# Performance work log

Hardware: AMD Instinct MI355X
Metric: run time of the kernel (lower is better)

## Reference

```python
import jax, jax.numpy as jnp
import numpy as np

N_NODES = 50000
N_EDGES = 640000
NFEAT = 128
NHID = 128
BN_EPS = 1e-5
GIN_EPS = 0.0  # GINConv default eps


def setup_inputs() -> dict:
    key = jax.random.key(0)
    ks = jax.random.split(key, 8)
    x = jax.random.normal(ks[0], (N_NODES, NFEAT), dtype=jnp.float32)
    edge_index = jax.random.randint(ks[1], (2, N_EDGES), 0, N_NODES, dtype=jnp.int64)
    # xavier-uniform linears, zero bias (per weights_init); BN gamma=1, beta=0
    def xavier(k, fan_in, fan_out):
        a = float(np.sqrt(6.0 / (fan_in + fan_out)))
        return jax.random.uniform(k, (fan_in, fan_out), dtype=jnp.float32, minval=-a, maxval=a)
    W1 = xavier(ks[2], NFEAT, NHID)
    b1 = jnp.zeros((NHID,), dtype=jnp.float32)
    gamma = jnp.ones((NHID,), dtype=jnp.float32)
    beta = jnp.zeros((NHID,), dtype=jnp.float32)
    W2 = xavier(ks[3], NHID, NHID)
    b2 = jnp.zeros((NHID,), dtype=jnp.float32)
    return {"x": x, "edge_index": edge_index, "W1": W1, "b1": b1,
            "gamma": gamma, "beta": beta, "W2": W2, "b2": b2}


def reference(x, edge_index, W1, b1, gamma, beta, W2, b2):
    src, dst = edge_index[0], edge_index[1]
    # sparse neighbor sum-aggregation: agg[i] = sum_{(src->dst=i)} x[src]
    agg = jax.ops.segment_sum(x[src], dst, num_segments=x.shape[0])
    h = (1.0 + GIN_EPS) * x + agg
    # MLP: Linear -> ReLU -> BatchNorm1d (training-mode batch stats) -> Linear
    h = jax.nn.relu(h @ W1 + b1)
    mean = jnp.mean(h, axis=0)
    var = jnp.mean(jnp.square(h - mean), axis=0)  # biased var, as torch BN uses
    h = (h - mean) * jax.lax.rsqrt(var + BN_EPS) * gamma + beta
    return h @ W2 + b2
```

## Files before the change

kernel.cpp:

```cpp
#include <hip/hip_runtime.h>
#include <hip/hip_fp16.h>

#define NNODES 50000
#define NEDGES 640000
#define NF 128
#define XB 3125
#define BINS 196
#define BINCAP 4096
#define P1B 157

typedef __attribute__((ext_vector_type(8))) _Float16 f16x8;
typedef __attribute__((ext_vector_type(4))) float f32x4;

__global__ __launch_bounds__(256) void k_prep(const float* __restrict__ x,
                                              const float* __restrict__ W1,
                                              unsigned short* __restrict__ xh,
                                              _Float16* __restrict__ wp1,
                                              int* __restrict__ gcursor,
                                              float* __restrict__ stats) {
  const int bid = blockIdx.x, t = threadIdx.x;
  if (bid < XB) {
    int i = bid * 256 + t;
    const float4 a = ((const float4*)x)[2 * i];
    const float4 b = ((const float4*)x)[2 * i + 1];
    __half2 h0 = __float22half2_rn(make_float2(a.x, a.y));
    __half2 h1 = __float22half2_rn(make_float2(a.z, a.w));
    __half2 h2 = __float22half2_rn(make_float2(b.x, b.y));
    __half2 h3 = __float22half2_rn(make_float2(b.z, b.w));
    uint4 v;
    v.x = *(unsigned*)&h0; v.y = *(unsigned*)&h1;
    v.z = *(unsigned*)&h2; v.w = *(unsigned*)&h3;
    ((uint4*)xh)[i] = v;
    if (bid == 0) {
      stats[t] = 0.f;
      stats[256 + t] = 0.f;
      if (t < BINS) gcursor[t] = 0;
    }
  } else {
    int f = (bid - XB) * 256 + t;
    int j = f & 7, lane = (f >> 3) & 63, cf = (f >> 9) & 7, ks = f >> 12;
    int k = ks * 32 + ((lane >> 4) << 3) + j;
    int n = cf * 16 + (lane & 15);
    float w = W1[k * NF + n];
    _Float16 hi = (_Float16)w;
    _Float16 lo = (_Float16)(w - (float)hi);
    wp1[f] = hi;
    wp1[16384 + f] = lo;
  }
}

__global__ __launch_bounds__(256) void k_p1(const int* __restrict__ ei,
                                            int* __restrict__ gcursor,
                                            unsigned* __restrict__ binbuf) {
  __shared__ int lcnt[BINS], lbase[BINS];
  const int t = threadIdx.x;
  const int e0 = blockIdx.x * 4096;
  const int n = min(4096, NEDGES - e0);
  if (t < BINS) lcnt[t] = 0;
  __syncthreads();
  for (int i = t; i < n; i += 256)
    atomicAdd(&lcnt[ei[NEDGES + e0 + i] >> 8], 1);
  __syncthreads();
  if (t < BINS) {
    lbase[t] = atomicAdd(&gcursor[t], lcnt[t]);
    lcnt[t] = 0;
  }
  __syncthreads();
  for (int i = t; i < n; i += 256) {
    int s = ei[e0 + i];
    int d = ei[NEDGES + e0 + i];
    int bin = d >> 8;
    int pos = atomicAdd(&lcnt[bin], 1);
    int idx = lbase[bin] + pos;
    if (idx < BINCAP)
      binbuf[bin * BINCAP + idx] = ((unsigned)(d & 255) << 16) | (unsigned)s;
  }
}

__global__ __launch_bounds__(256) void k_p2(const unsigned* __restrict__ binbuf,
                                            const int* __restrict__ gcursor,
                                            int* __restrict__ begdeg,
                                            unsigned short* __restrict__ slot) {
  __shared__ int cnt2[256], pst[256];
  __shared__ unsigned short stg[BINCAP];
  const int t = threadIdx.x;
  const int b = blockIdx.x;
  const int base = b * BINCAP;
  const int nb = min(gcursor[b], BINCAP);
  cnt2[t] = 0;
  __syncthreads();
  for (int i = t; i < nb; i += 256)
    atomicAdd(&cnt2[binbuf[base + i] >> 16], 1);
  __syncthreads();
  pst[t] = cnt2[t];
  __syncthreads();
  for (int d = 1; d < 256; d <<= 1) {
    int u = (t >= d) ? pst[t - d] : 0;
    __syncthreads();
    pst[t] += u;
    __syncthreads();
  }
  pst[t] -= cnt2[t];
  int node = (b << 8) + t;
  if (node < NNODES)
    begdeg[node] = ((base + pst[t]) << 8) | min(cnt2[t], 255);
  cnt2[t] = 0;
  __syncthreads();
  for (int i = t; i < nb; i += 256) {
    unsigned p = binbuf[base + i];
    int dl = p >> 16;
    int pos = atomicAdd(&cnt2[dl], 1);
    stg[pst[dl] + pos] = (unsigned short)(p & 0xffffu);
  }
  __syncthreads();
  for (int i = t; i < nb; i += 256) slot[base + i] = stg[i];
}

__device__ inline void add8h(float* a, uint4 v) {
  const __half2* p = (const __half2*)&v;
#pragma unroll
  for (int q = 0; q < 4; ++q) {
    float2 f = __half22float2(p[q]);
    a[2 * q] += f.x;
    a[2 * q + 1] += f.y;
  }
}

__global__ __launch_bounds__(256) void k_gather(const unsigned short* __restrict__ xh,
                                                const int* __restrict__ begdeg,
                                                const unsigned short* __restrict__ slot,
                                                _Float16* __restrict__ h) {
  const int t = threadIdx.x;
  const int wv = t >> 6, l = t & 63;
  const int node = blockIdx.x * 4 + wv;
  if (node >= NNODES) return;
  const int cg = (l & 15) << 3;
  const int e = l >> 4;
  const int bd = begdeg[node];
  const int beg = bd >> 8;
  const int end = beg + (bd & 255);
  float a[8] = {0.f, 0.f, 0.f, 0.f, 0.f, 0.f, 0.f, 0.f};
  float b[8] = {0.f, 0.f, 0.f, 0.f, 0.f, 0.f, 0.f, 0.f};
  int j = beg + e;
  for (; j + 4 < end; j += 8) {
    const uint4 v0 = *(const uint4*)(xh + (size_t)slot[j] * NF + cg);
    const uint4 v1 = *(const uint4*)(xh + (size_t)slot[j + 4] * NF + cg);
    add8h(a, v0);
    add8h(b, v1);
  }
  if (j < end) {
    const uint4 v0 = *(const uint4*)(xh + (size_t)slot[j] * NF + cg);
    add8h(a, v0);
  }
#pragma unroll
  for (int q = 0; q < 8; ++q) a[q] += b[q];
#pragma unroll
  for (int q = 0; q < 8; ++q) {
    a[q] += __shfl_xor(a[q], 16);
    a[q] += __shfl_xor(a[q], 32);
  }
  if (e == 0) {
    const uint4 sv = *(const uint4*)(xh + (size_t)node * NF + cg);
    add8h(a, sv);
    f16x8 o;
#pragma unroll
    for (int q = 0; q < 8; ++q) o[q] = (_Float16)a[q];
    *(f16x8*)(h + (size_t)node * NF + cg) = o;
  }
}

template <int MODE>
__global__ __launch_bounds__(256, 2) void k_gemm(const _Float16* __restrict__ A,
                                                 const _Float16* __restrict__ wprep,
                                                 const float* __restrict__ bias,
                                                 float* __restrict__ stats,
                                                 _Float16* __restrict__ outh,
                                                 float* __restrict__ outf) {
  __shared__ _Float16 wl[32768];
  __shared__ float red[2][4][128];

  const int t = threadIdx.x;
  const int wv = t >> 6;
  const int l = t & 63;
  const int wrow0 = blockIdx.x * 128 + wv * 16;

  f16x8 areg[2][4];
#pragma unroll
  for (int m = 0; m < 2; ++m) {
    const int arow = wrow0 + m * 64 + (l & 15);
    const bool okA = arow < NNODES;
#pragma unroll
    for (int ks = 0; ks < 4; ++ks) {
      if (okA) {
        areg[m][ks] = *(const f16x8*)(A + (size_t)arow * NF + ks * 32 + ((l >> 4) << 3));
      } else {
        areg[m][ks] = (f16x8){};
      }
    }
  }

  const float4* src = (const float4*)wprep;
#pragma unroll
  for (int it = 0; it < 16; ++it) {
    ((float4*)wl)[it * 256 + t] = src[it * 256 + t];
  }
  __syncthreads();

  f32x4 acc[2][8];
#pragma unroll
  for (int m = 0; m < 2; ++m)
#pragma unroll
    for (int cf = 0; cf < 8; ++cf) acc[m][cf] = (f32x4){0.f, 0.f, 0.f, 0.f};

#pragma unroll
  for (int ks = 0; ks < 4; ++ks) {
#pragma unroll
    for (int cf = 0; cf < 8; ++cf) {
      const int fo = (((ks * 8 + cf) << 6) + l) << 3;
      f16x8 bh = *(const f16x8*)(wl + fo);
      f16x8 bl = *(const f16x8*)(wl + 16384 + fo);
#pragma unroll
      for (int m = 0; m < 2; ++m) {
        acc[m][cf] = __builtin_amdgcn_mfma_f32_16x16x32_f16(areg[m][ks], bh, acc[m][cf], 0, 0, 0);
        acc[m][cf] = __builtin_amdgcn_mfma_f32_16x16x32_f16(areg[m][ks], bl, acc[m][cf], 0, 0, 0);
      }
    }
  }

  const int col16 = l & 15;
  const int rg = l >> 4;
  float bl_[8];
#pragma unroll
  for (int cf = 0; cf < 8; ++cf) bl_[cf] = bias[cf * 16 + col16];

  if (MODE == 0) {
    float cs[8], cq[8];
#pragma unroll
    for (int cf = 0; cf < 8; ++cf) { cs[cf] = 0.f; cq[cf] = 0.f; }
#pragma unroll
    for (int m = 0; m < 2; ++m)
#pragma unroll
      for (int cf = 0; cf < 8; ++cf) {
#pragma unroll
        for (int r = 0; r < 4; ++r) {
          int row = wrow0 + m * 64 + rg * 4 + r;
          if (row < NNODES) {
            float v = fmaxf(acc[m][cf][r] + bl_[cf], 0.f);
            outh[(size_t)row * NF + cf * 16 + col16] = (_Float16)v;
            cs[cf] += v;
            cq[cf] += v * v;
          }
        }
      }
#pragma unroll
    for (int cf = 0; cf < 8; ++cf) {
      cs[cf] += __shfl_xor(cs[cf], 16); cs[cf] += __shfl_xor(cs[cf], 32);
      cq[cf] += __shfl_xor(cq[cf], 16); cq[cf] += __shfl_xor(cq[cf], 32);
    }
    if (l < 16) {
#pragma unroll
      for (int cf = 0; cf < 8; ++cf) {
        red[0][wv][cf * 16 + l] = cs[cf];
        red[1][wv][cf * 16 + l] = cq[cf];
      }
    }
    __syncthreads();
    if (t < 128) {
      float s = red[0][0][t] + red[0][1][t] + red[0][2][t] + red[0][3][t];
      float q = red[1][0][t] + red[1][1][t] + red[1][2][t] + red[1][3][t];
      unsafeAtomicAdd(stats + t, s);
      unsafeAtomicAdd(stats + 128 + t, q);
    }
  } else {
#pragma unroll
    for (int m = 0; m < 2; ++m)
#pragma unroll
      for (int cf = 0; cf < 8; ++cf) {
#pragma unroll
        for (int r = 0; r < 4; ++r) {
          int row = wrow0 + m * 64 + rg * 4 + r;
          if (row < NNODES)
            outf[(size_t)row * NF + cf * 16 + col16] = acc[m][cf][r] + bl_[cf];
        }
      }
  }
}

__global__ __launch_bounds__(1024) void k_bnfold(const float* __restrict__ stats,
                                                 const float* __restrict__ gamma,
                                                 const float* __restrict__ beta,
                                                 const float* __restrict__ W2,
                                                 const float* __restrict__ b2,
                                                 _Float16* __restrict__ wp2,
                                                 float* __restrict__ b2p) {
  __shared__ float sc_s[128], sh_s[128];
  __shared__ float part[8][128];
  const int t = threadIdx.x;
  if (t < 128) {
    const float inv = 1.0f / (float)NNODES;
    float mean = stats[t] * inv;
    float var = stats[128 + t] * inv - mean * mean;
    var = fmaxf(var, 0.f);
    float sc = gamma[t] * rsqrtf(var + 1e-5f);
    sc_s[t] = sc;
    sh_s[t] = beta[t] - mean * sc;
  }
  __syncthreads();
#pragma unroll
  for (int it = 0; it < 16; ++it) {
    int f = it * 1024 + t;
    int j = f & 7, lane = (f >> 3) & 63, cf = (f >> 9) & 7, ks = f >> 12;
    int k = ks * 32 + ((lane >> 4) << 3) + j;
    int n = cf * 16 + (lane & 15);
    float w = sc_s[k] * W2[k * NF + n];
    _Float16 hi = (_Float16)w;
    _Float16 lo = (_Float16)(w - (float)hi);
    wp2[f] = hi;
    wp2[16384 + f] = lo;
  }
  {
    const int col = t & 127, ch = t >> 7;
    float s = 0.f;
    for (int k = ch * 16; k < ch * 16 + 16; ++k) s += sh_s[k] * W2[k * NF + col];
    part[ch][col] = s;
  }
  __syncthreads();
  if (t < 128) {
    float v = b2[t];
#pragma unroll
    for (int c = 0; c < 8; ++c) v += part[c][t];
    b2p[t] = v;
  }
}

extern "C" void kernel_launch(void* const* d_in, const int* in_sizes, int n_in,
                              void* d_out, int out_size, void* d_ws, size_t ws_size,
                              hipStream_t stream) {
  const float* x     = (const float*)d_in[0];
  const int*   ei    = (const int*)d_in[1];
  const float* W1    = (const float*)d_in[2];
  const float* b1    = (const float*)d_in[3];
  const float* gamma = (const float*)d_in[4];
  const float* beta  = (const float*)d_in[5];
  const float* W2    = (const float*)d_in[6];
  const float* b2    = (const float*)d_in[7];
  float* out = (float*)d_out;

  _Float16* h = (_Float16*)d_out;

  float*          stats   = (float*)d_ws;
  _Float16*       wp1     = (_Float16*)(stats + 512);
  _Float16*       wp2     = wp1 + 32768;
  float*          b2p     = (float*)(wp2 + 32768);
  int*            gcursor = (int*)(b2p + 128);
  int*            begdeg  = gcursor + 256;
  unsigned*       binbuf  = (unsigned*)(begdeg + 50176);
  unsigned short* slot    = (unsigned short*)(binbuf + BINS * BINCAP);
  unsigned short* xh      = slot + BINS * BINCAP;
  _Float16*       h1      = (_Float16*)(xh + (size_t)NNODES * NF);

  k_prep   <<<XB + 64, 256, 0, stream>>>(x, W1, xh, wp1, gcursor, stats);
  k_p1     <<<P1B, 256, 0, stream>>>(ei, gcursor, binbuf);
  k_p2     <<<BINS, 256, 0, stream>>>(binbuf, gcursor, begdeg, slot);
  k_gather <<<(NNODES + 3) / 4, 256, 0, stream>>>(xh, begdeg, slot, h);
  k_gemm<0><<<(NNODES + 127) / 128, 256, 0, stream>>>(h, wp1, b1, stats, h1, nullptr);
  k_bnfold <<<1, 1024, 0, stream>>>(stats, gamma, beta, W2, b2, wp2, b2p);
  k_gemm<1><<<(NNODES + 127) / 128, 256, 0, stream>>>(h1, wp2, b2p, nullptr, nullptr, out);
}
```

Baseline: 104.5 us.

## Fuse edge binning into prep kernel and register-cache bin entries in p2

Moves the edge-binning pass (k_p1) into k_prep as extra blocks, 1024 edges per block with vectorized int4 loads, so it runs concurrently with the fp16 conversion of x and W1 packing. Clearing gcursor now uses a hipMemsetAsync, since the binning blocks can no longer rely on block 0 of the same kernel to zero it. k_p2 loads up to 16 bin entries per thread into registers once and reuses them for both the count and scatter passes instead of reading binbuf twice. This removes one kernel launch and one global re-read but adds a memset call and more global atomics on gcursor, with 625 blocks instead of 157.

```diff
diff --git a/kernel.cpp b/kernel.cpp
--- a/kernel.cpp
+++ b/kernel.cpp
@@ -5,19 +5,23 @@
 #define NEDGES 640000
 #define NF 128
 #define XB 3125
+#define WB 64
 #define BINS 196
 #define BINCAP 4096
-#define P1B 157
+#define P1B 625
 
 typedef __attribute__((ext_vector_type(8))) _Float16 f16x8;
 typedef __attribute__((ext_vector_type(4))) float f32x4;
 
 __global__ __launch_bounds__(256) void k_prep(const float* __restrict__ x,
                                               const float* __restrict__ W1,
+                                              const int* __restrict__ ei,
                                               unsigned short* __restrict__ xh,
                                               _Float16* __restrict__ wp1,
                                               int* __restrict__ gcursor,
+                                              unsigned* __restrict__ binbuf,
                                               float* __restrict__ stats) {
+  __shared__ int lcnt[BINS], lbase[BINS];
   const int bid = blockIdx.x, t = threadIdx.x;
   if (bid < XB) {
     int i = bid * 256 + t;
@@ -31,12 +35,8 @@
     v.x = *(unsigned*)&h0; v.y = *(unsigned*)&h1;
     v.z = *(unsigned*)&h2; v.w = *(unsigned*)&h3;
     ((uint4*)xh)[i] = v;
-    if (bid == 0) {
-      stats[t] = 0.f;
-      stats[256 + t] = 0.f;
-      if (t < BINS) gcursor[t] = 0;
-    }
-  } else {
+    if (bid == 0) { stats[t] = 0.f; stats[256 + t] = 0.f; }
+  } else if (bid < XB + WB) {
     int f = (bid - XB) * 256 + t;
     int j = f & 7, lane = (f >> 3) & 63, cf = (f >> 9) & 7, ks = f >> 12;
     int k = ks * 32 + ((lane >> 4) << 3) + j;
@@ -46,34 +46,42 @@
     _Float16 lo = (_Float16)(w - (float)hi);
     wp1[f] = hi;
     wp1[16384 + f] = lo;
-  }
-}
-
-__global__ __launch_bounds__(256) void k_p1(const int* __restrict__ ei,
-                                            int* __restrict__ gcursor,
-                                            unsigned* __restrict__ binbuf) {
-  __shared__ int lcnt[BINS], lbase[BINS];
-  const int t = threadIdx.x;
-  const int e0 = blockIdx.x * 4096;
-  const int n = min(4096, NEDGES - e0);
-  if (t < BINS) lcnt[t] = 0;
-  __syncthreads();
-  for (int i = t; i < n; i += 256)
-    atomicAdd(&lcnt[ei[NEDGES + e0 + i] >> 8], 1);
-  __syncthreads();
-  if (t < BINS) {
-    lbase[t] = atomicAdd(&gcursor[t], lcnt[t]);
-    lcnt[t] = 0;
-  }
-  __syncthreads();
-  for (int i = t; i < n; i += 256) {
-    int s = ei[e0 + i];
-    int d = ei[NEDGES + e0 + i];
-    int bin = d >> 8;
-    int pos = atomicAdd(&lcnt[bin], 1);
-    int idx = lbase[bin] + pos;
-    if (idx < BINCAP)
-      binbuf[bin * BINCAP + idx] = ((unsigned)(d & 255) << 16) | (unsigned)s;
+  } else {
+    const int e0 = (bid - (XB + WB)) * 1024;
+    const int4 s4 = *(const int4*)(ei + e0 + 4 * t);
+    const int4 d4 = *(const int4*)(ei + NEDGES + e0 + 4 * t);
+    if (t < BINS) lcnt[t] = 0;
+    __syncthreads();
+    atomicAdd(&lcnt[d4.x >> 8], 1);
+    atomicAdd(&lcnt[d4.y >> 8], 1);
+    atomicAdd(&lcnt[d4.z >> 8], 1);
+    atomicAdd(&lcnt[d4.w >> 8], 1);
+    __syncthreads();
+    if (t < BINS) {
+      lbase[t] = atomicAdd(&gcursor[t], lcnt[t]);
+      lcnt[t] = 0;
+    }
+    __syncthreads();
+    {
+      int bin = d4.x >> 8;
+      int idx = lbase[bin] + atomicAdd(&lcnt[bin], 1);
+      if (idx < BINCAP) binbuf[bin * BINCAP + idx] = ((unsigned)(d4.x & 255) << 16) | (unsigned)s4.x;
+    }
+    {
+      int bin = d4.y >> 8;
+      int idx = lbase[bin] + atomicAdd(&lcnt[bin], 1);
+      if (idx < BINCAP) binbuf[bin * BINCAP + idx] = ((unsigned)(d4.y & 255) << 16) | (unsigned)s4.y;
+    }
+    {
+      int bin = d4.z >> 8;
+      int idx = lbase[bin] + atomicAdd(&lcnt[bin], 1);
+      if (idx < BINCAP) binbuf[bin * BINCAP + idx] = ((unsigned)(d4.z & 255) << 16) | (unsigned)s4.z;
+    }
+    {
+      int bin = d4.w >> 8;
+      int idx = lbase[bin] + atomicAdd(&lcnt[bin], 1);
+      if (idx < BINCAP) binbuf[bin * BINCAP + idx] = ((unsigned)(d4.w & 255) << 16) | (unsigned)s4.w;
+    }
   }
 }
 
@@ -87,10 +95,17 @@
   const int b = blockIdx.x;
   const int base = b * BINCAP;
   const int nb = min(gcursor[b], BINCAP);
+  unsigned pk[16];
+#pragma unroll
+  for (int ci = 0; ci < 16; ++ci) {
+    int i = (ci << 8) + t;
+    pk[ci] = (i < nb) ? binbuf[base + i] : 0xFFFFFFFFu;
+  }
   cnt2[t] = 0;
   __syncthreads();
-  for (int i = t; i < nb; i += 256)
-    atomicAdd(&cnt2[binbuf[base + i] >> 16], 1);
+#pragma unroll
+  for (int ci = 0; ci < 16; ++ci)
+    if (pk[ci] != 0xFFFFFFFFu) atomicAdd(&cnt2[(int)(pk[ci] >> 16)], 1);
   __syncthreads();
   pst[t] = cnt2[t];
   __syncthreads();
@@ -106,12 +121,13 @@
     begdeg[node] = ((base + pst[t]) << 8) | min(cnt2[t], 255);
   cnt2[t] = 0;
   __syncthreads();
-  for (int i = t; i < nb; i += 256) {
-    unsigned p = binbuf[base + i];
-    int dl = p >> 16;
-    int pos = atomicAdd(&cnt2[dl], 1);
-    stg[pst[dl] + pos] = (unsigned short)(p & 0xffffu);
-  }
+#pragma unroll
+  for (int ci = 0; ci < 16; ++ci)
+    if (pk[ci] != 0xFFFFFFFFu) {
+      int dl = (int)(pk[ci] >> 16);
+      int pos = atomicAdd(&cnt2[dl], 1);
+      stg[pst[dl] + pos] = (unsigned short)(pk[ci] & 0xffffu);
+    }
   __syncthreads();
   for (int i = t; i < nb; i += 256) slot[base + i] = stg[i];
 }
@@ -359,8 +375,8 @@
   unsigned short* xh      = slot + BINS * BINCAP;
   _Float16*       h1      = (_Float16*)(xh + (size_t)NNODES * NF);
 
-  k_prep   <<<XB + 64, 256, 0, stream>>>(x, W1, xh, wp1, gcursor, stats);
-  k_p1     <<<P1B, 256, 0, stream>>>(ei, gcursor, binbuf);
+  hipMemsetAsync(gcursor, 0, 256 * sizeof(int), stream);
+  k_prep   <<<XB + WB + P1B, 256, 0, stream>>>(x, W1, ei, xh, wp1, gcursor, binbuf, stats);
   k_p2     <<<BINS, 256, 0, stream>>>(binbuf, gcursor, begdeg, slot);
   k_gather <<<(NNODES + 3) / 4, 256, 0, stream>>>(xh, begdeg, slot, h);
   k_gemm<0><<<(NNODES + 127) / 128, 256, 0, stream>>>(h, wp1, b1, stats, h1, nullptr);
```

Result: no change. 105.3 us (+0.8%).
